# Optimization experiments

Hardware: AMD Instinct MI355X
Metric: run time of the kernel (lower is better)

Reference implementation:

```python
import jax, jax.numpy as jnp
import numpy as np

R = 16
ALPHA = 32
SCALING = ALPHA / R  # 2.0
E = 8
TOP_K = 2


def setup_inputs() -> dict:
    key = jax.random.key(0)
    ks = jax.random.split(key, 5)
    B, S, D = 4, 2048, 4096
    x = jax.random.normal(ks[0], (B, S, D), dtype=jnp.float32)
    base_W = jax.random.normal(ks[1], (D, D), dtype=jnp.float32) * 0.02
    router_W = jax.random.normal(ks[2], (E, D), dtype=jnp.float32) * 0.02
    lora_A = jax.random.normal(ks[3], (E, D, R), dtype=jnp.float32) * 0.02
    lora_B = jax.random.normal(ks[4], (E, R, D), dtype=jnp.float32) * 0.02
    return {"x": x, "base_W": base_W, "router_W": router_W,
            "lora_A": lora_A, "lora_B": lora_B}


def reference(x, base_W, router_W, lora_A, lora_B):
    # base linear: y = x @ W^T  (nn.Linear, bias=False)
    base = jnp.einsum('bsd,od->bso', x, base_W)

    # router logits and top-2 routing (softmax in fp32, as in torch)
    logits = jnp.einsum('bsd,ed->bse', x, router_W)
    probs = jax.nn.softmax(logits.astype(jnp.float32), axis=-1)  # [B,S,E]
    top_vals, top_idx = jax.lax.top_k(probs, TOP_K)               # [B,S,2]
    rw = top_vals / jnp.sum(top_vals, axis=-1, keepdims=True)
    # scatter top-2 weights into dense [B,S,E] combine matrix
    w_dense = jnp.sum(jax.nn.one_hot(top_idx, E, dtype=rw.dtype) * rw[..., None],
                      axis=-2).astype(x.dtype)                    # [B,S,E]

    # expert LoRA: out_n = sum_e w_ne * (x_n @ A_e @ B_e)
    # apply routing weight at rank-r stage (B_e linear => same math),
    # avoiding the [B,S,E,D] intermediate.
    mid = jnp.einsum('bsd,edr->bser', x, lora_A)                  # [B,S,E,r]
    mid = mid * w_dense[..., None]
    inc = jnp.einsum('bser,erd->bsd', mid, lora_B)                # [B,S,D]

    return base + inc * SCALING
```

## Files before the change

### kernel.cpp

```cpp
#include <hip/hip_runtime.h>
#include <math.h>

#define DI __device__ __forceinline__

typedef __attribute__((ext_vector_type(4))) float  f32x4;
typedef __attribute__((ext_vector_type(4))) short  s16x4;
typedef __attribute__((ext_vector_type(8))) short  s16x8;
typedef __attribute__((ext_vector_type(4))) float  ffrag;
typedef s16x8 bfrag;

constexpr int NT = 8192;
constexpr int D  = 4096;
constexpr int NE = 8;
constexpr int KE = 128;
constexpr int KX = D + KE;

DI short f2bf(float f) {
  unsigned u = __builtin_bit_cast(unsigned, f);
  u += 0x7FFFu + ((u >> 16) & 1u);
  return (short)(u >> 16);
}
DI float bf2f(short h) {
  unsigned u = ((unsigned)(unsigned short)h) << 16;
  return __builtin_bit_cast(float, u);
}

#define GLOAD16(gp, lp)                                                        \
  __builtin_amdgcn_global_load_lds(                                            \
      (const __attribute__((address_space(1))) void*)(gp),                     \
      (__attribute__((address_space(3))) void*)(lp), 16, 0, 0)

__global__ void moe_k_detect(const unsigned* __restrict__ x, int* __restrict__ flag) {
  int l = threadIdx.x;
  int cnt = 0;
  for (int i = l; i < 2048; i += 64) {
    unsigned e = (x[i] >> 23) & 0xFFu;
    cnt += (e >= 110u && e <= 140u) ? 1 : 0;
  }
#pragma unroll
  for (int o = 32; o; o >>= 1) cnt += __shfl_xor(cnt, o);
  if (l == 0) flag[0] = (cnt > 1024) ? 0 : 1;
}

__global__ __launch_bounds__(256)
void moe_k_prep_xr(const void* __restrict__ wp, const void* __restrict__ lAp,
                   const void* __restrict__ lBp, const void* __restrict__ xp,
                   const void* __restrict__ rp, const int* __restrict__ flag,
                   short* __restrict__ Wb, short* __restrict__ Abt,
                   short* __restrict__ Xb, float* __restrict__ wdense) {
  const bool bf = flag[0] != 0;
  int b = blockIdx.x, t = threadIdx.x;
  if (b < 8192) {
    int tid = b * 256 + t;
    int row = tid >> 9;
    int col = (tid & 511) << 3;
    s16x8 o;
    if (!bf) {
      const float* Wf = (const float*)wp;
      f32x4 v0 = *(const f32x4*)&Wf[(size_t)row * 4096 + col];
      f32x4 v1 = *(const f32x4*)&Wf[(size_t)row * 4096 + col + 4];
      o[0] = f2bf(v0[0]); o[1] = f2bf(v0[1]); o[2] = f2bf(v0[2]); o[3] = f2bf(v0[3]);
      o[4] = f2bf(v1[0]); o[5] = f2bf(v1[1]); o[6] = f2bf(v1[2]); o[7] = f2bf(v1[3]);
    } else {
      o = *(const s16x8*)&((const short*)wp)[(size_t)row * 4096 + col];
    }
    *(s16x8*)&Wb[(size_t)row * KX + col] = o;
  } else if (b < 8208) {
    int d = (b - 8192) * 256 + t;
    for (int j0 = 0; j0 < KE; j0 += 8) {
      s16x8 o;
#pragma unroll
      for (int i = 0; i < 8; ++i) {
        float v = bf ? bf2f(((const short*)lBp)[(size_t)(j0 + i) * 4096 + d])
                     : ((const float*)lBp)[(size_t)(j0 + i) * 4096 + d];
        o[i] = f2bf(2.0f * v);
      }
      *(s16x8*)&Wb[(size_t)d * KX + 4096 + j0] = o;
    }
  } else if (b < 8336) {
    int j = b - 8208;
    int e = j >> 4, r = j & 15;
    for (int d = t; d < 4096; d += 256) {
      size_t src = ((size_t)e * 4096 + d) * 16 + r;
      short v = bf ? ((const short*)lAp)[src] : f2bf(((const float*)lAp)[src]);
      Abt[(size_t)j * 4096 + d] = v;
    }
  } else {
    int wv = t >> 6, l = t & 63;
    int n = (b - 8336) * 4 + wv;
    float acc[NE];
#pragma unroll
    for (int e = 0; e < NE; ++e) acc[e] = 0.f;
    const float* xf = (const float*)xp;
    const short* xh = (const short*)xp;
    const float* rf = (const float*)rp;
    const short* rh = (const short*)rp;
    for (int it = 0; it < 16; ++it) {
      int d = it * 256 + l * 4;
      float x0, x1, x2, x3;
      s16x4 xo;
      if (!bf) {
        f32x4 v = *(const f32x4*)&xf[(size_t)n * D + d];
        x0 = v[0]; x1 = v[1]; x2 = v[2]; x3 = v[3];
        xo[0] = f2bf(x0); xo[1] = f2bf(x1); xo[2] = f2bf(x2); xo[3] = f2bf(x3);
      } else {
        xo = *(const s16x4*)&xh[(size_t)n * D + d];
        x0 = bf2f(xo[0]); x1 = bf2f(xo[1]); x2 = bf2f(xo[2]); x3 = bf2f(xo[3]);
      }
      *(s16x4*)&Xb[(size_t)n * KX + d] = xo;
#pragma unroll
      for (int e = 0; e < NE; ++e) {
        if (!bf) {
          f32x4 w = *(const f32x4*)&rf[(size_t)e * D + d];
          acc[e] += x0 * w[0] + x1 * w[1] + x2 * w[2] + x3 * w[3];
        } else {
          s16x4 w = *(const s16x4*)&rh[(size_t)e * D + d];
          acc[e] += x0 * bf2f(w[0]) + x1 * bf2f(w[1]) + x2 * bf2f(w[2]) + x3 * bf2f(w[3]);
        }
      }
    }
#pragma unroll
    for (int e = 0; e < NE; ++e) {
#pragma unroll
      for (int o = 32; o; o >>= 1) acc[e] += __shfl_xor(acc[e], o);
    }
    float m = acc[0];
#pragma unroll
    for (int e = 1; e < NE; ++e) m = fmaxf(m, acc[e]);
    float p[NE];
#pragma unroll
    for (int e = 0; e < NE; ++e) p[e] = __expf(acc[e] - m);
    int i1 = 0; float v1 = p[0];
#pragma unroll
    for (int e = 1; e < NE; ++e) { if (p[e] > v1) { v1 = p[e]; i1 = e; } }
    int i2 = 0; float v2 = -1.f;
#pragma unroll
    for (int e = 0; e < NE; ++e) { if (e != i1 && p[e] > v2) { v2 = p[e]; i2 = e; } }
    float inv = 1.f / (v1 + v2);
    if (l < NE) {
      float w = (l == i1) ? v1 * inv : ((l == i2) ? v2 * inv : 0.f);
      wdense[(size_t)n * NE + l] = w;
    }
  }
}

__global__ __launch_bounds__(256)
void moe_k_mid2(const short* __restrict__ Xb, const short* __restrict__ Abt,
                const float* __restrict__ wdense, short* __restrict__ XbW) {
  __shared__ __align__(16) short LDS[16384];
  const int t = threadIdx.x, l = t & 63, wv = t >> 6;
  const int wr = wv >> 1, wc = wv & 1;
  const int lr = l & 15, kq = l >> 4;
  const int m0 = (blockIdx.x >> 1) * 64;
  const int j0 = (blockIdx.x & 1) * 64;

  ffrag acc[2][2];
#pragma unroll
  for (int i = 0; i < 2; ++i)
#pragma unroll
    for (int j = 0; j < 2; ++j)
#pragma unroll
      for (int q = 0; q < 4; ++q) acc[i][j][q] = 0.f;

  const int srow = t >> 2, sslot = t & 3;
#define MSTAGE(kt_)                                                            \
  do {                                                                         \
    int _k0 = (kt_) * 32, _b = ((kt_) & 3) * 4096;                             \
    GLOAD16(&Xb[(size_t)(m0 + srow) * KX + _k0 + sslot * 8], &LDS[_b + t * 8]);\
    GLOAD16(&Abt[(size_t)(j0 + srow) * 4096 + _k0 + sslot * 8],                \
            &LDS[_b + 2048 + t * 8]);                                          \
  } while (0)

  MSTAGE(0); MSTAGE(1); MSTAGE(2);
  constexpr int NKT = 128;

  for (int kt = 0; kt < NKT; ++kt) {
    if (kt + 2 < NKT)      asm volatile("s_waitcnt vmcnt(4)" ::: "memory");
    else if (kt + 1 < NKT) asm volatile("s_waitcnt vmcnt(2)" ::: "memory");
    else                   asm volatile("s_waitcnt vmcnt(0)" ::: "memory");
    __builtin_amdgcn_s_barrier();
    __builtin_amdgcn_sched_barrier(0);

    const int bufs = (kt & 3) * 4096;
    const short* As = &LDS[bufs + (wr * 32 + lr) * 32 + kq * 8];
    const short* Bs = &LDS[bufs + 2048 + (wc * 32 + lr) * 32 + kq * 8];
    bfrag a0 = *(const bfrag*)&As[0];
    bfrag a1 = *(const bfrag*)&As[512];
    bfrag b0 = *(const bfrag*)&Bs[0];
    bfrag b1 = *(const bfrag*)&Bs[512];
    if (kt + 3 < NKT) MSTAGE(kt + 3);
    asm volatile("" ::: "memory");
    acc[0][0] = __builtin_amdgcn_mfma_f32_16x16x32_bf16(b0, a0, acc[0][0], 0, 0, 0);
    acc[0][1] = __builtin_amdgcn_mfma_f32_16x16x32_bf16(b1, a0, acc[0][1], 0, 0, 0);
    acc[1][0] = __builtin_amdgcn_mfma_f32_16x16x32_bf16(b0, a1, acc[1][0], 0, 0, 0);
    acc[1][1] = __builtin_amdgcn_mfma_f32_16x16x32_bf16(b1, a1, acc[1][1], 0, 0, 0);
  }

#pragma unroll
  for (int m = 0; m < 2; ++m)
#pragma unroll
    for (int n = 0; n < 2; ++n) {
      int gr = m0 + wr * 32 + m * 16 + lr;
      int jb = j0 + wc * 32 + n * 16 + kq * 4;
      int e  = jb >> 4;
      float w = wdense[(size_t)gr * NE + e];
      s16x4 o;
#pragma unroll
      for (int q = 0; q < 4; ++q) o[q] = f2bf(acc[m][n][q] * w);
      *(s16x4*)&XbW[(size_t)gr * KX + 4096 + jb] = o;
    }
#undef MSTAGE
}

__global__ __launch_bounds__(512, 2)
void moe_k_main8(const short* __restrict__ Xb, const short* __restrict__ Wb,
                 const int* __restrict__ flag, void* __restrict__ outp) {
  __shared__ __align__(16) short LDS[65536];
  const int t = threadIdx.x;
  const int l = t & 63;
  const int wv = t >> 6;
  const int wr = wv >> 2;
  const int wc = wv & 3;
  const int lr = l & 15;
  const int kq = l >> 4;

  int wg = blockIdx.x;
  int swz = (wg & 7) * 64 + (wg >> 3);
  const int tm = (swz >> 4) * 256;
  const int tn = (swz & 15) * 256;

  ffrag acc[8][4];
#pragma unroll
  for (int i = 0; i < 8; ++i)
#pragma unroll
    for (int j = 0; j < 4; ++j)
#pragma unroll
      for (int q = 0; q < 4; ++q) acc[i][j][q] = 0.f;

#define STAGE_ONE(kt_, base_, src_, half_)                                     \
  do {                                                                         \
    int _k0 = (kt_) * 32, _b = ((kt_) & 3) * 16384 + (base_);                  \
    int _c = (half_) * 512 + t;                                                \
    int _r = _c >> 2;                                                          \
    int _kc = (_c & 3) ^ ((_r >> 1) & 3);                                      \
    GLOAD16(&src_[(size_t)((base_ ? tn : tm) + _r) * KX + _k0 + _kc * 8],      \
            &LDS[_b + _c * 8]);                                                \
  } while (0)
#define STAGE_A1(kt_) STAGE_ONE(kt_, 0,    Xb, 0)
#define STAGE_A2(kt_) STAGE_ONE(kt_, 0,    Xb, 1)
#define STAGE_B1(kt_) STAGE_ONE(kt_, 8192, Wb, 0)
#define STAGE_B2(kt_) STAGE_ONE(kt_, 8192, Wb, 1)

  STAGE_A1(0); STAGE_A2(0); STAGE_B1(0); STAGE_B2(0);
  STAGE_A1(1); STAGE_A2(1); STAGE_B1(1); STAGE_B2(1);
  STAGE_A1(2); STAGE_A2(2); STAGE_B1(2); STAGE_B2(2);

  constexpr int NKT = KX / 32;

  const int kx = kq ^ ((lr >> 1) & 3);
  const int aofs = (wr * 128 + lr) * 32 + kx * 8;
  const int bofs = 8192 + (wc * 64 + lr) * 32 + kx * 8;

#define MFMA1(m_, n_, av_, bv_)                                                \
  acc[m_][n_] = __builtin_amdgcn_mfma_f32_16x16x32_bf16(bv_, av_, acc[m_][n_], 0, 0, 0);

  for (int kt = 0; kt < NKT; ++kt) {
    if (kt + 2 < NKT)      asm volatile("s_waitcnt vmcnt(8)" ::: "memory");
    else if (kt + 1 < NKT) asm volatile("s_waitcnt vmcnt(4)" ::: "memory");
    else                   asm volatile("s_waitcnt vmcnt(0)" ::: "memory");
    __builtin_amdgcn_s_barrier();
    __builtin_amdgcn_sched_barrier(0);

    const int bufs = (kt & 3) * 16384;
    const short* Ab = &LDS[bufs + aofs];
    const short* Bb = &LDS[bufs + bofs];

    bfrag b0 = *(const bfrag*)&Bb[0];
    bfrag b1 = *(const bfrag*)&Bb[512];
    bfrag a0 = *(const bfrag*)&Ab[0];
    bfrag a1 = *(const bfrag*)&Ab[512];
    bfrag a2 = *(const bfrag*)&Ab[1024];
    bfrag a3 = *(const bfrag*)&Ab[1536];
    if (kt + 3 < NKT) STAGE_A1(kt + 3);
    __builtin_amdgcn_s_barrier();
    asm volatile("s_waitcnt lgkmcnt(0)" ::: "memory");
    __builtin_amdgcn_sched_barrier(0);
    __builtin_amdgcn_s_setprio(1);
    MFMA1(0, 0, a0, b0) MFMA1(0, 1, a0, b1)
    MFMA1(1, 0, a1, b0) MFMA1(1, 1, a1, b1)
    MFMA1(2, 0, a2, b0) MFMA1(2, 1, a2, b1)
    MFMA1(3, 0, a3, b0) MFMA1(3, 1, a3, b1)
    __builtin_amdgcn_s_setprio(0);
    __builtin_amdgcn_sched_barrier(0);

    bfrag a4 = *(const bfrag*)&Ab[2048];
    bfrag a5 = *(const bfrag*)&Ab[2560];
    bfrag a6 = *(const bfrag*)&Ab[3072];
    bfrag a7 = *(const bfrag*)&Ab[3584];
    if (kt + 3 < NKT) STAGE_A2(kt + 3);
    __builtin_amdgcn_s_barrier();
    asm volatile("s_waitcnt lgkmcnt(0)" ::: "memory");
    __builtin_amdgcn_sched_barrier(0);
    __builtin_amdgcn_s_setprio(1);
    MFMA1(4, 0, a4, b0) MFMA1(4, 1, a4, b1)
    MFMA1(5, 0, a5, b0) MFMA1(5, 1, a5, b1)
    MFMA1(6, 0, a6, b0) MFMA1(6, 1, a6, b1)
    MFMA1(7, 0, a7, b0) MFMA1(7, 1, a7, b1)
    __builtin_amdgcn_s_setprio(0);
    __builtin_amdgcn_sched_barrier(0);

    bfrag b2 = *(const bfrag*)&Bb[1024];
    bfrag b3 = *(const bfrag*)&Bb[1536];
    if (kt + 3 < NKT) STAGE_B1(kt + 3);
    __builtin_amdgcn_s_barrier();
    asm volatile("s_waitcnt lgkmcnt(0)" ::: "memory");
    __builtin_amdgcn_sched_barrier(0);
    __builtin_amdgcn_s_setprio(1);
    MFMA1(4, 2, a4, b2) MFMA1(4, 3, a4, b3)
    MFMA1(5, 2, a5, b2) MFMA1(5, 3, a5, b3)
    MFMA1(6, 2, a6, b2) MFMA1(6, 3, a6, b3)
    MFMA1(7, 2, a7, b2) MFMA1(7, 3, a7, b3)
    __builtin_amdgcn_s_setprio(0);
    __builtin_amdgcn_sched_barrier(0);

    if (kt + 3 < NKT) STAGE_B2(kt + 3);
    __builtin_amdgcn_s_setprio(1);
    MFMA1(0, 2, a0, b2) MFMA1(0, 3, a0, b3)
    MFMA1(1, 2, a1, b2) MFMA1(1, 3, a1, b3)
    MFMA1(2, 2, a2, b2) MFMA1(2, 3, a2, b3)
    MFMA1(3, 2, a3, b2) MFMA1(3, 3, a3, b3)
    __builtin_amdgcn_s_setprio(0);
    __builtin_amdgcn_sched_barrier(0);
  }

  const bool bf = flag[0] != 0;
  float* of = (float*)outp;
  unsigned short* oh = (unsigned short*)outp;
#pragma unroll
  for (int m = 0; m < 8; ++m)
#pragma unroll
    for (int n = 0; n < 4; ++n) {
      int gr = tm + wr * 128 + m * 16 + lr;
      int gc = tn + wc * 64 + n * 16 + kq * 4;
      if (!bf) {
        *(f32x4*)&of[(size_t)gr * D + gc] = acc[m][n];
      } else {
        s16x4 o;
#pragma unroll
        for (int q = 0; q < 4; ++q) o[q] = f2bf(acc[m][n][q]);
        *(s16x4*)&oh[(size_t)gr * D + gc] = o;
      }
    }
#undef STAGE_ONE
#undef STAGE_A1
#undef STAGE_A2
#undef STAGE_B1
#undef STAGE_B2
#undef MFMA1
}

extern "C" void kernel_launch(void* const* d_in, const int* in_sizes, int n_in,
                              void* d_out, int out_size, void* d_ws, size_t ws_size,
                              hipStream_t stream) {
  const void* x  = d_in[0];
  const void* bw = d_in[1];
  const void* rw = d_in[2];
  const void* lA = d_in[3];
  const void* lB = d_in[4];

  char* ws = (char*)d_ws;
  const size_t XB_BYTES  = (size_t)NT * KX * 2;
  const size_t WB_BYTES  = (size_t)D * KX * 2;
  const size_t ABT_BYTES = (size_t)KE * D * 2;
  const size_t WD_BYTES  = (size_t)NT * NE * 4;
  const size_t NEED = 256 + XB_BYTES + WB_BYTES + ABT_BYTES + WD_BYTES;
  if (ws_size < NEED) return;

  int*   flag   = (int*)ws;
  short* Xb     = (short*)(ws + 256);
  short* Wb     = (short*)(ws + 256 + XB_BYTES);
  short* Abt    = (short*)(ws + 256 + XB_BYTES + WB_BYTES);
  float* wdense = (float*)(ws + 256 + XB_BYTES + WB_BYTES + ABT_BYTES);

  hipLaunchKernelGGL(moe_k_detect, dim3(1), dim3(64), 0, stream,
                     (const unsigned*)x, flag);
  hipLaunchKernelGGL(moe_k_prep_xr, dim3(10384), dim3(256), 0, stream,
                     bw, lA, lB, x, rw, flag, Wb, Abt, Xb, wdense);
  hipLaunchKernelGGL(moe_k_mid2, dim3(256), dim3(256), 0, stream,
                     Xb, Abt, wdense, Xb);
  hipLaunchKernelGGL(moe_k_main8, dim3(512), dim3(512), 0, stream,
                     Xb, Wb, flag, d_out);
}
```

Baseline: 394.1 us.

## Restructure main GEMM pipeline to double-buffered 64-wide K tiles

Changes the main GEMM K-loop from a four-stage ring of 32-wide K tiles to a two-buffer scheme with 64-wide K tiles, each split into two 32-wide sub-stages. Each phase now issues 16 MFMAs over all four B fragments, which halves the loop iterations and the per-iteration barrier and waitcnt overhead. Global-to-LDS staging of the next tile is interleaved across the four phases. The cost is a shallower prefetch distance, so memory latency may be less well hidden, and the added barriers per phase and vmcnt bookkeeping could stall.

```diff
diff --git a/kernel.cpp b/kernel.cpp
--- a/kernel.cpp
+++ b/kernel.cpp
@@ -213,7 +213,7 @@
 }
 
 __global__ __launch_bounds__(512, 2)
-void moe_k_main8(const short* __restrict__ Xb, const short* __restrict__ Wb,
+void moe_k_main9(const short* __restrict__ Xb, const short* __restrict__ Wb,
                  const int* __restrict__ flag, void* __restrict__ outp) {
   __shared__ __align__(16) short LDS[65536];
   const int t = threadIdx.x;
@@ -237,100 +237,110 @@
 #pragma unroll
       for (int q = 0; q < 4; ++q) acc[i][j][q] = 0.f;
 
-#define STAGE_ONE(kt_, base_, src_, half_)                                     \
+  constexpr int NKT = KX / 64;
+
+#define SU(kt_, REG_, src_, tb_, h_, ks_)                                      \
   do {                                                                         \
-    int _k0 = (kt_) * 32, _b = ((kt_) & 3) * 16384 + (base_);                  \
-    int _c = (half_) * 512 + t;                                                \
-    int _r = _c >> 2;                                                          \
-    int _kc = (_c & 3) ^ ((_r >> 1) & 3);                                      \
-    GLOAD16(&src_[(size_t)((base_ ? tn : tm) + _r) * KX + _k0 + _kc * 8],      \
-            &LDS[_b + _c * 8]);                                                \
+    int _rp = t >> 2;                                                          \
+    int _kc = (t & 3) ^ ((_rp >> 1) & 3);                                      \
+    GLOAD16(&src_[(size_t)((tb_) + (h_) * 128 + _rp) * KX +                    \
+                  (kt_) * 64 + (ks_) * 32 + _kc * 8],                          \
+            &LDS[((kt_) & 1) * 32768 + (REG_) + (ks_) * 8192 +                 \
+                 (h_) * 4096 + t * 8]);                                        \
   } while (0)
-#define STAGE_A1(kt_) STAGE_ONE(kt_, 0,    Xb, 0)
-#define STAGE_A2(kt_) STAGE_ONE(kt_, 0,    Xb, 1)
-#define STAGE_B1(kt_) STAGE_ONE(kt_, 8192, Wb, 0)
-#define STAGE_B2(kt_) STAGE_ONE(kt_, 8192, Wb, 1)
-
-  STAGE_A1(0); STAGE_A2(0); STAGE_B1(0); STAGE_B2(0);
-  STAGE_A1(1); STAGE_A2(1); STAGE_B1(1); STAGE_B2(1);
-  STAGE_A1(2); STAGE_A2(2); STAGE_B1(2); STAGE_B2(2);
-
-  constexpr int NKT = KX / 32;
+#define SU_A(kt_, h_, ks_) SU(kt_, 0,     Xb, tm, h_, ks_)
+#define SU_B(kt_, h_, ks_) SU(kt_, 16384, Wb, tn, h_, ks_)
+
+  SU_A(0, 0, 0); SU_A(0, 1, 0); SU_B(0, 0, 0); SU_B(0, 1, 0);
+  SU_A(0, 0, 1); SU_A(0, 1, 1); SU_B(0, 0, 1); SU_B(0, 1, 1);
+  SU_A(1, 0, 0); SU_A(1, 1, 0); SU_B(1, 0, 0); SU_B(1, 1, 0);
+  asm volatile("s_waitcnt vmcnt(8)" ::: "memory");
+  __builtin_amdgcn_s_barrier();
+  asm volatile("" ::: "memory");
 
   const int kx = kq ^ ((lr >> 1) & 3);
-  const int aofs = (wr * 128 + lr) * 32 + kx * 8;
-  const int bofs = 8192 + (wc * 64 + lr) * 32 + kx * 8;
-
-#define MFMA1(m_, n_, av_, bv_)                                                \
+  const int abase = (wr * 128 + lr) * 32 + kx * 8;
+  const int bbase = 16384 + (wc * 64 + lr) * 32 + kx * 8;
+
+#define MM(m_, n_, bv_, av_)                                                   \
   acc[m_][n_] = __builtin_amdgcn_mfma_f32_16x16x32_bf16(bv_, av_, acc[m_][n_], 0, 0, 0);
 
+#define PH_TOP()                                                               \
+  __builtin_amdgcn_s_barrier();                                                \
+  asm volatile("s_waitcnt lgkmcnt(0)" ::: "memory");                           \
+  __builtin_amdgcn_sched_barrier(0);                                           \
+  __builtin_amdgcn_s_setprio(1);
+#define PH_END()                                                               \
+  __builtin_amdgcn_s_setprio(0);                                               \
+  __builtin_amdgcn_s_barrier();                                                \
+  asm volatile("" ::: "memory");
+
   for (int kt = 0; kt < NKT; ++kt) {
-    if (kt + 2 < NKT)      asm volatile("s_waitcnt vmcnt(8)" ::: "memory");
-    else if (kt + 1 < NKT) asm volatile("s_waitcnt vmcnt(4)" ::: "memory");
-    else                   asm volatile("s_waitcnt vmcnt(0)" ::: "memory");
-    __builtin_amdgcn_s_barrier();
-    __builtin_amdgcn_sched_barrier(0);
-
-    const int bufs = (kt & 3) * 16384;
-    const short* Ab = &LDS[bufs + aofs];
-    const short* Bb = &LDS[bufs + bofs];
-
-    bfrag b0 = *(const bfrag*)&Bb[0];
-    bfrag b1 = *(const bfrag*)&Bb[512];
-    bfrag a0 = *(const bfrag*)&Ab[0];
-    bfrag a1 = *(const bfrag*)&Ab[512];
-    bfrag a2 = *(const bfrag*)&Ab[1024];
-    bfrag a3 = *(const bfrag*)&Ab[1536];
-    if (kt + 3 < NKT) STAGE_A1(kt + 3);
-    __builtin_amdgcn_s_barrier();
-    asm volatile("s_waitcnt lgkmcnt(0)" ::: "memory");
-    __builtin_amdgcn_sched_barrier(0);
-    __builtin_amdgcn_s_setprio(1);
-    MFMA1(0, 0, a0, b0) MFMA1(0, 1, a0, b1)
-    MFMA1(1, 0, a1, b0) MFMA1(1, 1, a1, b1)
-    MFMA1(2, 0, a2, b0) MFMA1(2, 1, a2, b1)
-    MFMA1(3, 0, a3, b0) MFMA1(3, 1, a3, b1)
-    __builtin_amdgcn_s_setprio(0);
-    __builtin_amdgcn_sched_barrier(0);
-
-    bfrag a4 = *(const bfrag*)&Ab[2048];
-    bfrag a5 = *(const bfrag*)&Ab[2560];
-    bfrag a6 = *(const bfrag*)&Ab[3072];
-    bfrag a7 = *(const bfrag*)&Ab[3584];
-    if (kt + 3 < NKT) STAGE_A2(kt + 3);
-    __builtin_amdgcn_s_barrier();
-    asm volatile("s_waitcnt lgkmcnt(0)" ::: "memory");
-    __builtin_amdgcn_sched_barrier(0);
-    __builtin_amdgcn_s_setprio(1);
-    MFMA1(4, 0, a4, b0) MFMA1(4, 1, a4, b1)
-    MFMA1(5, 0, a5, b0) MFMA1(5, 1, a5, b1)
-    MFMA1(6, 0, a6, b0) MFMA1(6, 1, a6, b1)
-    MFMA1(7, 0, a7, b0) MFMA1(7, 1, a7, b1)
-    __builtin_amdgcn_s_setprio(0);
-    __builtin_amdgcn_sched_barrier(0);
-
-    bfrag b2 = *(const bfrag*)&Bb[1024];
-    bfrag b3 = *(const bfrag*)&Bb[1536];
-    if (kt + 3 < NKT) STAGE_B1(kt + 3);
-    __builtin_amdgcn_s_barrier();
-    asm volatile("s_waitcnt lgkmcnt(0)" ::: "memory");
-    __builtin_amdgcn_sched_barrier(0);
-    __builtin_amdgcn_s_setprio(1);
-    MFMA1(4, 2, a4, b2) MFMA1(4, 3, a4, b3)
-    MFMA1(5, 2, a5, b2) MFMA1(5, 3, a5, b3)
-    MFMA1(6, 2, a6, b2) MFMA1(6, 3, a6, b3)
-    MFMA1(7, 2, a7, b2) MFMA1(7, 3, a7, b3)
-    __builtin_amdgcn_s_setprio(0);
-    __builtin_amdgcn_sched_barrier(0);
-
-    if (kt + 3 < NKT) STAGE_B2(kt + 3);
-    __builtin_amdgcn_s_setprio(1);
-    MFMA1(0, 2, a0, b2) MFMA1(0, 3, a0, b3)
-    MFMA1(1, 2, a1, b2) MFMA1(1, 3, a1, b3)
-    MFMA1(2, 2, a2, b2) MFMA1(2, 3, a2, b3)
-    MFMA1(3, 2, a3, b2) MFMA1(3, 3, a3, b3)
-    __builtin_amdgcn_s_setprio(0);
-    __builtin_amdgcn_sched_barrier(0);
+    const int bufS = (kt & 1) * 32768;
+    const short* Ap = &LDS[bufS + abase];
+    const short* Bp = &LDS[bufS + bbase];
+    const bool more = (kt + 1 < NKT);
+
+    bfrag b0 = *(const bfrag*)&Bp[0];
+    bfrag b1 = *(const bfrag*)&Bp[512];
+    bfrag b2 = *(const bfrag*)&Bp[1024];
+    bfrag b3 = *(const bfrag*)&Bp[1536];
+    bfrag a0 = *(const bfrag*)&Ap[0];
+    bfrag a1 = *(const bfrag*)&Ap[512];
+    bfrag a2 = *(const bfrag*)&Ap[1024];
+    bfrag a3 = *(const bfrag*)&Ap[1536];
+    if (more && kt > 0) { SU_A(kt + 1, 0, 0); SU_A(kt + 1, 1, 0); }
+    PH_TOP()
+    MM(0, 0, b0, a0) MM(0, 1, b1, a0) MM(0, 2, b2, a0) MM(0, 3, b3, a0)
+    MM(1, 0, b0, a1) MM(1, 1, b1, a1) MM(1, 2, b2, a1) MM(1, 3, b3, a1)
+    MM(2, 0, b0, a2) MM(2, 1, b1, a2) MM(2, 2, b2, a2) MM(2, 3, b3, a2)
+    MM(3, 0, b0, a3) MM(3, 1, b1, a3) MM(3, 2, b2, a3) MM(3, 3, b3, a3)
+    PH_END()
+
+    bfrag a4 = *(const bfrag*)&Ap[2048];
+    bfrag a5 = *(const bfrag*)&Ap[2560];
+    bfrag a6 = *(const bfrag*)&Ap[3072];
+    bfrag a7 = *(const bfrag*)&Ap[3584];
+    if (more && kt > 0) { SU_B(kt + 1, 0, 0); SU_B(kt + 1, 1, 0); }
+    if (more) asm volatile("s_waitcnt vmcnt(4)" ::: "memory");
+    else      asm volatile("s_waitcnt vmcnt(0)" ::: "memory");
+    PH_TOP()
+    MM(4, 0, b0, a4) MM(4, 1, b1, a4) MM(4, 2, b2, a4) MM(4, 3, b3, a4)
+    MM(5, 0, b0, a5) MM(5, 1, b1, a5) MM(5, 2, b2, a5) MM(5, 3, b3, a5)
+    MM(6, 0, b0, a6) MM(6, 1, b1, a6) MM(6, 2, b2, a6) MM(6, 3, b3, a6)
+    MM(7, 0, b0, a7) MM(7, 1, b1, a7) MM(7, 2, b2, a7) MM(7, 3, b3, a7)
+    PH_END()
+
+    const short* Aq = Ap + 8192;
+    const short* Bq = Bp + 8192;
+    bfrag c0 = *(const bfrag*)&Bq[0];
+    bfrag c1 = *(const bfrag*)&Bq[512];
+    bfrag c2 = *(const bfrag*)&Bq[1024];
+    bfrag c3 = *(const bfrag*)&Bq[1536];
+    bfrag e4 = *(const bfrag*)&Aq[2048];
+    bfrag e5 = *(const bfrag*)&Aq[2560];
+    bfrag e6 = *(const bfrag*)&Aq[3072];
+    bfrag e7 = *(const bfrag*)&Aq[3584];
+    if (more) { SU_A(kt + 1, 0, 1); SU_A(kt + 1, 1, 1); }
+    PH_TOP()
+    MM(4, 0, c0, e4) MM(4, 1, c1, e4) MM(4, 2, c2, e4) MM(4, 3, c3, e4)
+    MM(5, 0, c0, e5) MM(5, 1, c1, e5) MM(5, 2, c2, e5) MM(5, 3, c3, e5)
+    MM(6, 0, c0, e6) MM(6, 1, c1, e6) MM(6, 2, c2, e6) MM(6, 3, c3, e6)
+    MM(7, 0, c0, e7) MM(7, 1, c1, e7) MM(7, 2, c2, e7) MM(7, 3, c3, e7)
+    PH_END()
+
+    bfrag e0 = *(const bfrag*)&Aq[0];
+    bfrag e1 = *(const bfrag*)&Aq[512];
+    bfrag e2 = *(const bfrag*)&Aq[1024];
+    bfrag e3 = *(const bfrag*)&Aq[1536];
+    if (more) { SU_B(kt + 1, 0, 1); SU_B(kt + 1, 1, 1); }
+    if (more) asm volatile("s_waitcnt vmcnt(4)" ::: "memory");
+    PH_TOP()
+    MM(0, 0, c0, e0) MM(0, 1, c1, e0) MM(0, 2, c2, e0) MM(0, 3, c3, e0)
+    MM(1, 0, c0, e1) MM(1, 1, c1, e1) MM(1, 2, c2, e1) MM(1, 3, c3, e1)
+    MM(2, 0, c0, e2) MM(2, 1, c1, e2) MM(2, 2, c2, e2) MM(2, 3, c3, e2)
+    MM(3, 0, c0, e3) MM(3, 1, c1, e3) MM(3, 2, c2, e3) MM(3, 3, c3, e3)
+    PH_END()
   }
 
   const bool bf = flag[0] != 0;
@@ -351,12 +361,12 @@
         *(s16x4*)&oh[(size_t)gr * D + gc] = o;
       }
     }
-#undef STAGE_ONE
-#undef STAGE_A1
-#undef STAGE_A2
-#undef STAGE_B1
-#undef STAGE_B2
-#undef MFMA1
+#undef SU
+#undef SU_A
+#undef SU_B
+#undef MM
+#undef PH_TOP
+#undef PH_END
 }
 
 extern "C" void kernel_launch(void* const* d_in, const int* in_sizes, int n_in,
@@ -388,6 +398,6 @@
                      bw, lA, lB, x, rw, flag, Wb, Abt, Xb, wdense);
   hipLaunchKernelGGL(moe_k_mid2, dim3(256), dim3(256), 0, stream,
                      Xb, Abt, wdense, Xb);
-  hipLaunchKernelGGL(moe_k_main8, dim3(512), dim3(512), 0, stream,
+  hipLaunchKernelGGL(moe_k_main9, dim3(512), dim3(512), 0, stream,
                      Xb, Wb, flag, d_out);
 }
```

Measured after the change: 394.3 us. No clear change (+0.0%).
